# Kernel optimization log

Hardware: AMD Instinct MI355X
Metric: run time of the kernel (lower is better)

The kernel has to match this reference:

```python
import jax, jax.numpy as jnp
import numpy as np

D_MODEL = 256
NUM_HEADS = 4
HEAD_DIM = D_MODEL // NUM_HEADS


def setup_inputs() -> dict:
    key = jax.random.key(0)
    ks = jax.random.split(key, 16)
    B, N, M, C = 2, 256, 256, D_MODEL
    inp = {
        'q_tokens': jax.random.normal(ks[0], (B, N, C), jnp.float32),
        'k_tokens': jax.random.normal(ks[1], (B, M, C), jnp.float32),
        'v_tokens': jax.random.normal(ks[2], (B, M, C), jnp.float32),
        'qk_embeds': jax.random.normal(ks[3], (B, N, M, C), jnp.float32),
        'qv_embeds': jax.random.normal(ks[4], (B, N, M, C), jnp.float32),
    }
    scale = 1.0 / np.sqrt(C)
    # Linear layer params (weight used as x @ W + b)
    inp['Wq'] = jax.random.normal(ks[5], (C, C), jnp.float32) * scale
    inp['bq'] = jnp.zeros((C,), jnp.float32)
    inp['Wk'] = jax.random.normal(ks[6], (C, C), jnp.float32) * scale
    inp['bk'] = jnp.zeros((C,), jnp.float32)
    inp['Wv'] = jax.random.normal(ks[7], (C, C), jnp.float32) * scale
    inp['bv'] = jnp.zeros((C,), jnp.float32)
    inp['Wqk'] = jax.random.normal(ks[8], (C, C), jnp.float32) * scale
    inp['bqk'] = jnp.zeros((C,), jnp.float32)
    inp['Wqv'] = jax.random.normal(ks[9], (C, C), jnp.float32) * scale
    inp['bqv'] = jnp.zeros((C,), jnp.float32)
    return inp


def reference(q_tokens, k_tokens, v_tokens, qk_embeds, qv_embeds,
              Wq, bq, Wk, bk, Wv, bv, Wqk, bqk, Wqv, bqv):
    B, N, C = q_tokens.shape
    M = k_tokens.shape[1]
    H, hc = NUM_HEADS, HEAD_DIM

    # token projections -> (B, H, len, hc)
    q = (q_tokens @ Wq + bq).reshape(B, N, H, hc).transpose(0, 2, 1, 3)
    k = (k_tokens @ Wk + bk).reshape(B, M, H, hc).transpose(0, 2, 1, 3)
    v = (v_tokens @ Wv + bv).reshape(B, M, H, hc).transpose(0, 2, 1, 3)

    # pair-embedding projections -> (B, N, M, H, hc)
    qk = (qk_embeds @ Wqk + bqk).reshape(B, N, M, H, hc)
    qv = (qv_embeds @ Wqv + bqv).reshape(B, N, M, H, hc)

    # scores: q . (k + qk)  == q.k + q.qk
    scores = jnp.einsum('bhnc,bhmc->bhnm', q, k)
    scores = scores + jnp.einsum('bhnc,bnmhc->bhnm', q, qk)
    scores = scores / np.sqrt(hc).astype(np.float32)

    attn = jax.nn.softmax(scores, axis=-1)  # (B, H, N, M)

    # output: attn @ (v + qv) == attn@v + attn.qv
    hidden = jnp.einsum('bhnm,bhmc->bhnc', attn, v)
    hidden = hidden + jnp.einsum('bhnm,bnmhc->bhnc', attn, qv)
    hidden = hidden.transpose(0, 2, 1, 3).reshape(B, N, C)  # (B, N, C)
    return hidden, attn
```

## Files before the change

### kernel.cpp

```cpp
#include <hip/hip_runtime.h>

#define BB 2
#define NN 256
#define CC 256

__device__ __forceinline__ float dot4acc(float4 e, float4 w, float s) {
    s = fmaf(e.x, w.x, s); s = fmaf(e.y, w.y, s);
    s = fmaf(e.z, w.z, s); s = fmaf(e.w, w.w, s);
    return s;
}

__global__ __launch_bounds__(256) void proj_gemm(
    const float* __restrict__ q_tok, const float* __restrict__ k_tok, const float* __restrict__ v_tok,
    const float* __restrict__ Wq, const float* __restrict__ bq,
    const float* __restrict__ Wk, const float* __restrict__ bk,
    const float* __restrict__ Wv, const float* __restrict__ bv,
    float* __restrict__ out)
{
    const int row0 = blockIdx.x * 64;
    const int col0 = blockIdx.y * 64;
    const int seg  = row0 >> 9;
    const float* A    = seg == 0 ? q_tok : (seg == 1 ? k_tok : v_tok);
    const float* W    = seg == 0 ? Wq    : (seg == 1 ? Wk    : Wv);
    const float* bias = seg == 0 ? bq    : (seg == 1 ? bk    : bv);
    const int ar0 = row0 & 511;

    __shared__ float As[64][17];
    __shared__ float Bs[16][68];
    const int t  = threadIdx.x;
    const int tr = t >> 4, tc = t & 15;
    float acc[4][4] = {};

    const int sr  = t >> 2, sk4 = (t & 3) << 2;
    const int bkr = t >> 4, bj4 = (t & 15) << 2;

    for (int k0 = 0; k0 < 256; k0 += 16) {
        float4 a4 = *reinterpret_cast<const float4*>(&A[(ar0 + sr) * 256 + k0 + sk4]);
        float4 b4 = *reinterpret_cast<const float4*>(&W[(k0 + bkr) * 256 + col0 + bj4]);
        As[sr][sk4 + 0] = a4.x; As[sr][sk4 + 1] = a4.y; As[sr][sk4 + 2] = a4.z; As[sr][sk4 + 3] = a4.w;
        Bs[bkr][bj4 + 0] = b4.x; Bs[bkr][bj4 + 1] = b4.y; Bs[bkr][bj4 + 2] = b4.z; Bs[bkr][bj4 + 3] = b4.w;
        __syncthreads();
        #pragma unroll
        for (int k = 0; k < 16; ++k) {
            float a[4], bbv[4];
            #pragma unroll
            for (int i = 0; i < 4; ++i) a[i] = As[tr * 4 + i][k];
            #pragma unroll
            for (int j = 0; j < 4; ++j) bbv[j] = Bs[k][tc * 4 + j];
            #pragma unroll
            for (int i = 0; i < 4; ++i)
                #pragma unroll
                for (int j = 0; j < 4; ++j)
                    acc[i][j] = fmaf(a[i], bbv[j], acc[i][j]);
        }
        __syncthreads();
    }
    #pragma unroll
    for (int i = 0; i < 4; ++i) {
        const int r = row0 + tr * 4 + i;
        #pragma unroll
        for (int j = 0; j < 4; ++j) {
            const int cj = col0 + tc * 4 + j;
            out[r * 256 + cj] = acc[i][j] + bias[cj];
        }
    }
}

__global__ __launch_bounds__(256) void qw_gemm(
    const float* __restrict__ qp, const float* __restrict__ Wqk, float* __restrict__ qW)
{
    const int h    = blockIdx.z;
    const int row0 = blockIdx.x * 64;
    const int d0   = blockIdx.y * 64;
    __shared__ float As[64][17];
    __shared__ float Bs[16][68];
    const int t  = threadIdx.x;
    const int tr = t >> 4, tc = t & 15;
    float acc[4][4] = {};
    const int sr = t >> 2, sc4 = (t & 3) << 2;

    for (int k0 = 0; k0 < 64; k0 += 16) {
        float4 a4 = *reinterpret_cast<const float4*>(&qp[(row0 + sr) * 256 + h * 64 + k0 + sc4]);
        float4 b4 = *reinterpret_cast<const float4*>(&Wqk[(d0 + sr) * 256 + h * 64 + k0 + sc4]);
        As[sr][sc4 + 0] = a4.x; As[sr][sc4 + 1] = a4.y; As[sr][sc4 + 2] = a4.z; As[sr][sc4 + 3] = a4.w;
        Bs[sc4 + 0][sr] = b4.x; Bs[sc4 + 1][sr] = b4.y; Bs[sc4 + 2][sr] = b4.z; Bs[sc4 + 3][sr] = b4.w;
        __syncthreads();
        #pragma unroll
        for (int k = 0; k < 16; ++k) {
            float a[4], bbv[4];
            #pragma unroll
            for (int i = 0; i < 4; ++i) a[i] = As[tr * 4 + i][k];
            #pragma unroll
            for (int j = 0; j < 4; ++j) bbv[j] = Bs[k][tc * 4 + j];
            #pragma unroll
            for (int i = 0; i < 4; ++i)
                #pragma unroll
                for (int j = 0; j < 4; ++j)
                    acc[i][j] = fmaf(a[i], bbv[j], acc[i][j]);
        }
        __syncthreads();
    }
    #pragma unroll
    for (int i = 0; i < 4; ++i)
        #pragma unroll
        for (int j = 0; j < 4; ++j)
            qW[((row0 + tr * 4 + i) * 4 + h) * 256 + d0 + tc * 4 + j] = acc[i][j];
}

__global__ __launch_bounds__(256) void qk_gemm(
    const float* __restrict__ qkvp, float* __restrict__ Sqk)
{
    const int bh = blockIdx.z;
    const int b  = bh >> 2, h = bh & 3;
    const int n0 = blockIdx.x * 64;
    const int m0 = blockIdx.y * 64;
    __shared__ float As[64][17];
    __shared__ float Bs[16][68];
    const int t  = threadIdx.x;
    const int tr = t >> 4, tc = t & 15;
    float acc[4][4] = {};
    const int sr = t >> 2, sc4 = (t & 3) << 2;

    for (int k0 = 0; k0 < 64; k0 += 16) {
        float4 a4 = *reinterpret_cast<const float4*>(&qkvp[(size_t)(b * 256 + n0 + sr) * 256 + h * 64 + k0 + sc4]);
        float4 b4 = *reinterpret_cast<const float4*>(&qkvp[(size_t)(512 + b * 256 + m0 + sr) * 256 + h * 64 + k0 + sc4]);
        As[sr][sc4 + 0] = a4.x; As[sr][sc4 + 1] = a4.y; As[sr][sc4 + 2] = a4.z; As[sr][sc4 + 3] = a4.w;
        Bs[sc4 + 0][sr] = b4.x; Bs[sc4 + 1][sr] = b4.y; Bs[sc4 + 2][sr] = b4.z; Bs[sc4 + 3][sr] = b4.w;
        __syncthreads();
        #pragma unroll
        for (int k = 0; k < 16; ++k) {
            float a[4], bbv[4];
            #pragma unroll
            for (int i = 0; i < 4; ++i) a[i] = As[tr * 4 + i][k];
            #pragma unroll
            for (int j = 0; j < 4; ++j) bbv[j] = Bs[k][tc * 4 + j];
            #pragma unroll
            for (int i = 0; i < 4; ++i)
                #pragma unroll
                for (int j = 0; j < 4; ++j)
                    acc[i][j] = fmaf(a[i], bbv[j], acc[i][j]);
        }
        __syncthreads();
    }
    #pragma unroll
    for (int i = 0; i < 4; ++i)
        #pragma unroll
        for (int j = 0; j < 4; ++j)
            Sqk[(size_t)((b * 4 + h) * 256 + n0 + tr * 4 + i) * 256 + m0 + tc * 4 + j] = acc[i][j];
}


#define S1_LOAD(E00,E01,E02,E03,E10,E11,E12,E13, MB)                          \
    do {                                                                      \
        const float* _r0 = qk_emb + (size_t)(bn * 256 + (MB) + lr) * 256 + lq * 4; \
        const float* _r1 = _r0 + 1024;                                        \
        E00 = *reinterpret_cast<const float4*>(_r0);                          \
        E01 = *reinterpret_cast<const float4*>(_r0 + 64);                     \
        E02 = *reinterpret_cast<const float4*>(_r0 + 128);                    \
        E03 = *reinterpret_cast<const float4*>(_r0 + 192);                    \
        E10 = *reinterpret_cast<const float4*>(_r1);                          \
        E11 = *reinterpret_cast<const float4*>(_r1 + 64);                     \
        E12 = *reinterpret_cast<const float4*>(_r1 + 128);                    \
        E13 = *reinterpret_cast<const float4*>(_r1 + 192);                    \
    } while (0)

#define S1_COMP(E00,E01,E02,E03,E10,E11,E12,E13, MB)                          \
    do {                                                                      \
        const int _m0 = (MB) + lr;                                            \
        float p0[4], p1[4];                                                   \
        _Pragma("unroll")                                                     \
        for (int hh = 0; hh < 4; ++hh) {                                      \
            const float4 w0 = *reinterpret_cast<const float4*>(&qWs[hh * 256 + lq * 4]);        \
            const float4 w1 = *reinterpret_cast<const float4*>(&qWs[hh * 256 + 64 + lq * 4]);   \
            const float4 w2 = *reinterpret_cast<const float4*>(&qWs[hh * 256 + 128 + lq * 4]);  \
            const float4 w3 = *reinterpret_cast<const float4*>(&qWs[hh * 256 + 192 + lq * 4]);  \
            float s0 = 0.f, s1 = 0.f;                                         \
            s0 = dot4acc(E00, w0, s0); s0 = dot4acc(E01, w1, s0);             \
            s0 = dot4acc(E02, w2, s0); s0 = dot4acc(E03, w3, s0);             \
            s1 = dot4acc(E10, w0, s1); s1 = dot4acc(E11, w1, s1);             \
            s1 = dot4acc(E12, w2, s1); s1 = dot4acc(E13, w3, s1);             \
            p0[hh] = s0; p1[hh] = s1;                                         \
        }                                                                     \
        _Pragma("unroll")                                                     \
        for (int hh = 0; hh < 4; ++hh) {                                      \
            p0[hh] += __shfl_xor(p0[hh], 1); p1[hh] += __shfl_xor(p1[hh], 1); \
            p0[hh] += __shfl_xor(p0[hh], 2); p1[hh] += __shfl_xor(p1[hh], 2); \
            p0[hh] += __shfl_xor(p0[hh], 4); p1[hh] += __shfl_xor(p1[hh], 4); \
            p0[hh] += __shfl_xor(p0[hh], 8); p1[hh] += __shfl_xor(p1[hh], 8); \
        }                                                                     \
        if (lq == 0) {                                                        \
            _Pragma("unroll")                                                 \
            for (int hh = 0; hh < 4; ++hh) {                                  \
                Ssc[hh * 256 + _m0]     = p0[hh];                             \
                Ssc[hh * 256 + _m0 + 4] = p1[hh];                             \
            }                                                                 \
        }                                                                     \
    } while (0)

#define S2_LOAD(F0,F1,F2,F3,F4,F5,F6,F7, MB)                                  \
    do {                                                                      \
        const float* _rb = qv_emb + (size_t)(bn * 256 + (MB)) * 256 + l * 4;  \
        F0 = *reinterpret_cast<const float4*>(_rb);                           \
        F1 = *reinterpret_cast<const float4*>(_rb + 256);                     \
        F2 = *reinterpret_cast<const float4*>(_rb + 512);                     \
        F3 = *reinterpret_cast<const float4*>(_rb + 768);                     \
        F4 = *reinterpret_cast<const float4*>(_rb + 1024);                    \
        F5 = *reinterpret_cast<const float4*>(_rb + 1280);                    \
        F6 = *reinterpret_cast<const float4*>(_rb + 1536);                    \
        F7 = *reinterpret_cast<const float4*>(_rb + 1792);                    \
    } while (0)

#define S2_ONE(F, RIDX)                                                       \
    do {                                                                      \
        _Pragma("unroll")                                                     \
        for (int hh = 0; hh < 4; ++hh) {                                      \
            const float a = attn_s[hh * 256 + (RIDX)];                        \
            acc[hh].x = fmaf(a, F.x, acc[hh].x);                              \
            acc[hh].y = fmaf(a, F.y, acc[hh].y);                              \
            acc[hh].z = fmaf(a, F.z, acc[hh].z);                              \
            acc[hh].w = fmaf(a, F.w, acc[hh].w);                              \
        }                                                                     \
    } while (0)

#define S2_COMP(F0,F1,F2,F3,F4,F5,F6,F7, MB)                                  \
    do {                                                                      \
        S2_ONE(F0, (MB) + 0); S2_ONE(F1, (MB) + 1);                           \
        S2_ONE(F2, (MB) + 2); S2_ONE(F3, (MB) + 3);                           \
        S2_ONE(F4, (MB) + 4); S2_ONE(F5, (MB) + 5);                           \
        S2_ONE(F6, (MB) + 6); S2_ONE(F7, (MB) + 7);                           \
    } while (0)

__global__ __launch_bounds__(512, 4) void mega4(
    const float* __restrict__ qk_emb, const float* __restrict__ qv_emb,
    const float* __restrict__ qkvp, const float* __restrict__ qW,
    const float* __restrict__ Sqk, const float* __restrict__ Wqv,
    const float* __restrict__ bqv,
    float* __restrict__ attn_out, float* __restrict__ hidden)
{
    const int bn = blockIdx.x;
    const int b  = bn >> 8, n = bn & 255;
    const int t  = threadIdx.x;
    const int w  = t >> 6, l = t & 63;

    __shared__ float qWs[1024];
    __shared__ float SqkL[1024];
    __shared__ float Ssc[1024];
    __shared__ float attn_s[1024];
    __shared__ float Ap[4096];
    __shared__ float stage[16][256];
    __shared__ float pr[2][256];
    __shared__ float mxs[8][4], sums[8][4], scl[8][4];

    if (t < 256)
        *reinterpret_cast<float4*>(&qWs[t * 4]) =
            *reinterpret_cast<const float4*>(&qW[(size_t)bn * 1024 + t * 4]);
    __syncthreads();

    const int lq = l & 15, lr = l >> 4, li = l & 31;
    const int mw = w * 32;

    if (l < 32) {
        #pragma unroll
        for (int h = 0; h < 4; ++h)
            SqkL[h * 256 + mw + li] =
                Sqk[(size_t)((b * 4 + h) * 256 + n) * 256 + mw + li];
    }

    {
        float4 a00, a01, a02, a03, a10, a11, a12, a13;
        float4 b00, b01, b02, b03, b10, b11, b12, b13;
        S1_LOAD(a00,a01,a02,a03,a10,a11,a12,a13, mw + 0);
        S1_LOAD(b00,b01,b02,b03,b10,b11,b12,b13, mw + 8);
        S1_COMP(a00,a01,a02,a03,a10,a11,a12,a13, mw + 0);
        S1_LOAD(a00,a01,a02,a03,a10,a11,a12,a13, mw + 16);
        S1_COMP(b00,b01,b02,b03,b10,b11,b12,b13, mw + 8);
        S1_LOAD(b00,b01,b02,b03,b10,b11,b12,b13, mw + 24);
        S1_COMP(a00,a01,a02,a03,a10,a11,a12,a13, mw + 16);
        S1_COMP(b00,b01,b02,b03,b10,b11,b12,b13, mw + 24);
    }

    float mxw[4], smw[4];
    #pragma unroll
    for (int h = 0; h < 4; ++h) {
        const float sc = (Ssc[h * 256 + mw + li] + SqkL[h * 256 + mw + li]) * 0.125f;
        float mx = sc;
        #pragma unroll
        for (int mask = 16; mask >= 1; mask >>= 1) mx = fmaxf(mx, __shfl_xor(mx, mask));
        const float e = __expf(sc - mx);
        attn_s[h * 256 + mw + li] = e;
        float sm = e;
        #pragma unroll
        for (int mask = 16; mask >= 1; mask >>= 1) sm += __shfl_xor(sm, mask);
        mxw[h] = mx; smw[h] = sm;
    }
    if (l == 0) {
        #pragma unroll
        for (int h = 0; h < 4; ++h) { mxs[w][h] = mxw[h]; sums[w][h] = smw[h]; }
    }

    float4 acc[4];
    #pragma unroll
    for (int hh = 0; hh < 4; ++hh) acc[hh] = make_float4(0.f, 0.f, 0.f, 0.f);
    {
        float4 f0, f1, f2, f3, f4, f5, f6, f7;
        float4 g0, g1, g2, g3, g4, g5, g6, g7;
        S2_LOAD(f0,f1,f2,f3,f4,f5,f6,f7, mw + 0);
        S2_LOAD(g0,g1,g2,g3,g4,g5,g6,g7, mw + 8);
        S2_COMP(f0,f1,f2,f3,f4,f5,f6,f7, mw + 0);
        S2_LOAD(f0,f1,f2,f3,f4,f5,f6,f7, mw + 16);
        S2_COMP(g0,g1,g2,g3,g4,g5,g6,g7, mw + 8);
        S2_LOAD(g0,g1,g2,g3,g4,g5,g6,g7, mw + 24);
        S2_COMP(f0,f1,f2,f3,f4,f5,f6,f7, mw + 16);
        S2_COMP(g0,g1,g2,g3,g4,g5,g6,g7, mw + 24);
    }
    __syncthreads();

    if (t < 4) {
        const int h = t;
        float mg = mxs[0][h];
        #pragma unroll
        for (int ww = 1; ww < 8; ++ww) mg = fmaxf(mg, mxs[ww][h]);
        float sr[8]; float sg = 0.f;
        #pragma unroll
        for (int ww = 0; ww < 8; ++ww) { sr[ww] = __expf(mxs[ww][h] - mg); sg += sums[ww][h] * sr[ww]; }
        const float inv = 1.f / sg;
        #pragma unroll
        for (int ww = 0; ww < 8; ++ww) scl[ww][h] = sr[ww] * inv;
    }
    __syncthreads();

    {
        const int h = t >> 7, j = t & 127;
        float* ao = attn_out + (size_t)((b * 4 + h) * 256 + n) * 256;
        #pragma unroll
        for (int rep = 0; rep < 2; ++rep) {
            const int jj = j + rep * 128;
            const float a = attn_s[h * 256 + jj] * scl[jj >> 5][h];
            attn_s[h * 256 + jj] = a;
            ao[jj] = a;
        }
    }
    if (w < 4) {
        #pragma unroll
        for (int hh = 0; hh < 4; ++hh) {
            const float s = scl[w][hh];
            float4 v = acc[hh];
            v.x *= s; v.y *= s; v.z *= s; v.w *= s;
            *reinterpret_cast<float4*>(&Ap[(w * 4 + hh) * 256 + l * 4]) = v;
        }
    }
    __syncthreads();
    if (w >= 4) {
        #pragma unroll
        for (int hh = 0; hh < 4; ++hh) {
            const float s = scl[w][hh];
            float4* p = reinterpret_cast<float4*>(&Ap[((w - 4) * 4 + hh) * 256 + l * 4]);
            float4 o = *p;
            o.x = fmaf(acc[hh].x, s, o.x); o.y = fmaf(acc[hh].y, s, o.y);
            o.z = fmaf(acc[hh].z, s, o.z); o.w = fmaf(acc[hh].w, s, o.w);
            *p = o;
        }
    }
    __syncthreads();
    #pragma unroll
    for (int i = 0; i < 2; ++i) {
        const int idx = t + i * 512;
        const int hh = idx >> 8, d = idx & 255;
        Ap[hh * 256 + d] = Ap[hh * 256 + d] + Ap[(4 + hh) * 256 + d]
                         + Ap[(8 + hh) * 256 + d] + Ap[(12 + hh) * 256 + d];
    }

    {
        const int c = t & 255, half = t >> 8, hc = c >> 6;
        const int fr0 = t >> 6, fc0 = (t & 63) * 4;
        const int fr1 = fr0 + 8;
        const float* vbase = qkvp + (size_t)(1024 + b * 256) * 256;
        float4 ra = *reinterpret_cast<const float4*>(&vbase[(size_t)fr0 * 256 + fc0]);
        float4 rb = *reinterpret_cast<const float4*>(&vbase[(size_t)fr1 * 256 + fc0]);
        float hv = 0.f;
        for (int mt = 0; mt < 16; ++mt) {
            __syncthreads();
            *reinterpret_cast<float4*>(&stage[fr0][fc0]) = ra;
            *reinterpret_cast<float4*>(&stage[fr1][fc0]) = rb;
            if (mt < 15) {
                ra = *reinterpret_cast<const float4*>(&vbase[(size_t)((mt + 1) * 16 + fr0) * 256 + fc0]);
                rb = *reinterpret_cast<const float4*>(&vbase[(size_t)((mt + 1) * 16 + fr1) * 256 + fc0]);
            } else {
                ra = *reinterpret_cast<const float4*>(&Wqv[(size_t)fr0 * 256 + fc0]);
                rb = *reinterpret_cast<const float4*>(&Wqv[(size_t)fr1 * 256 + fc0]);
            }
            __syncthreads();
            #pragma unroll
            for (int r = 0; r < 8; ++r)
                hv = fmaf(attn_s[hc * 256 + mt * 16 + half * 8 + r], stage[half * 8 + r][c], hv);
        }
        for (int dt = 0; dt < 16; ++dt) {
            __syncthreads();
            *reinterpret_cast<float4*>(&stage[fr0][fc0]) = ra;
            *reinterpret_cast<float4*>(&stage[fr1][fc0]) = rb;
            if (dt < 15) {
                ra = *reinterpret_cast<const float4*>(&Wqv[(size_t)((dt + 1) * 16 + fr0) * 256 + fc0]);
                rb = *reinterpret_cast<const float4*>(&Wqv[(size_t)((dt + 1) * 16 + fr1) * 256 + fc0]);
            }
            __syncthreads();
            #pragma unroll
            for (int r = 0; r < 8; ++r)
                hv = fmaf(Ap[hc * 256 + dt * 16 + half * 8 + r], stage[half * 8 + r][c], hv);
        }
        pr[half][c] = hv;
    }
    __syncthreads();
    if (t < 256)
        hidden[(size_t)bn * 256 + t] = pr[0][t] + pr[1][t] + bqv[t];
}

extern "C" void kernel_launch(void* const* d_in, const int* in_sizes, int n_in,
                              void* d_out, int out_size, void* d_ws, size_t ws_size,
                              hipStream_t stream) {
    (void)in_sizes; (void)n_in; (void)out_size; (void)ws_size;
    const float* q_tok  = (const float*)d_in[0];
    const float* k_tok  = (const float*)d_in[1];
    const float* v_tok  = (const float*)d_in[2];
    const float* qk_emb = (const float*)d_in[3];
    const float* qv_emb = (const float*)d_in[4];
    const float* Wq  = (const float*)d_in[5];   const float* bq  = (const float*)d_in[6];
    const float* Wk  = (const float*)d_in[7];   const float* bk  = (const float*)d_in[8];
    const float* Wv  = (const float*)d_in[9];   const float* bv  = (const float*)d_in[10];
    const float* Wqk = (const float*)d_in[11];
    const float* Wqv = (const float*)d_in[13];  const float* bqv = (const float*)d_in[14];

    float* ws   = (float*)d_ws;
    float* qkvp = ws;
    float* qW   = ws + 393216;
    float* Sqk  = ws + 917504;

    float* hidden = (float*)d_out;
    float* attn   = (float*)d_out + BB * NN * CC;

    proj_gemm<<<dim3(24, 4),   256, 0, stream>>>(q_tok, k_tok, v_tok, Wq, bq, Wk, bk, Wv, bv, qkvp);
    qw_gemm  <<<dim3(8, 4, 4), 256, 0, stream>>>(qkvp, Wqk, qW);
    qk_gemm  <<<dim3(4, 4, 8), 256, 0, stream>>>(qkvp, Sqk);
    mega4    <<<512,           512, 0, stream>>>(qk_emb, qv_emb, qkvp, qW, Sqk, Wqv, bqv, attn, hidden);
}
```

Measured before the change: 91.64 us.

## Split per-row output projection out of mega kernel into a batched tiled GEMM

The per-row attn@v and Afull@Wqv products, which each block computed by streaming all of v and Wqv through shared memory, move into a separate tiled GEMM kernel. mega5 now writes the aggregated attention-weighted qv embeddings to workspace, and out_gemm reads them back. Softmax rescaling is recomputed per thread instead of through an extra barrier-separated stage, and the Ap reduction now covers all 8 waves at once. This removes redundant per-block reads of v/Wqv and several barriers, at the cost of an extra launch and a global round trip for Afull and attn.

```diff
diff --git a/kernel.cpp b/kernel.cpp
--- a/kernel.cpp
+++ b/kernel.cpp
@@ -188,12 +188,10 @@
             p0[hh] += __shfl_xor(p0[hh], 4); p1[hh] += __shfl_xor(p1[hh], 4); \
             p0[hh] += __shfl_xor(p0[hh], 8); p1[hh] += __shfl_xor(p1[hh], 8); \
         }                                                                     \
-        if (lq == 0) {                                                        \
-            _Pragma("unroll")                                                 \
-            for (int hh = 0; hh < 4; ++hh) {                                  \
-                Ssc[hh * 256 + _m0]     = p0[hh];                             \
-                Ssc[hh * 256 + _m0 + 4] = p1[hh];                             \
-            }                                                                 \
+        _Pragma("unroll")                                                     \
+        for (int hh = 0; hh < 4; ++hh) {                                      \
+            Ssc[hh * 256 + _m0]     = p0[hh];                                 \
+            Ssc[hh * 256 + _m0 + 4] = p1[hh];                                 \
         }                                                                     \
     } while (0)
 
@@ -230,12 +228,10 @@
         S2_ONE(F6, (MB) + 6); S2_ONE(F7, (MB) + 7);                           \
     } while (0)
 
-__global__ __launch_bounds__(512, 4) void mega4(
+__global__ __launch_bounds__(512, 4) void mega5(
     const float* __restrict__ qk_emb, const float* __restrict__ qv_emb,
-    const float* __restrict__ qkvp, const float* __restrict__ qW,
-    const float* __restrict__ Sqk, const float* __restrict__ Wqv,
-    const float* __restrict__ bqv,
-    float* __restrict__ attn_out, float* __restrict__ hidden)
+    const float* __restrict__ qW, const float* __restrict__ Sqk,
+    float* __restrict__ attn_out, float* __restrict__ Afull_g)
 {
     const int bn = blockIdx.x;
     const int b  = bn >> 8, n = bn & 255;
@@ -246,25 +242,21 @@
     __shared__ float SqkL[1024];
     __shared__ float Ssc[1024];
     __shared__ float attn_s[1024];
-    __shared__ float Ap[4096];
-    __shared__ float stage[16][256];
-    __shared__ float pr[2][256];
-    __shared__ float mxs[8][4], sums[8][4], scl[8][4];
-
-    if (t < 256)
-        *reinterpret_cast<float4*>(&qWs[t * 4]) =
-            *reinterpret_cast<const float4*>(&qW[(size_t)bn * 1024 + t * 4]);
+    __shared__ float Ap[8192];
+    __shared__ float mxs[8][4], sums[8][4];
+
+    {
+        const int i2 = t * 2;
+        *reinterpret_cast<float2*>(&qWs[i2]) =
+            *reinterpret_cast<const float2*>(&qW[(size_t)bn * 1024 + i2]);
+        const int h = i2 >> 8, m = i2 & 255;
+        *reinterpret_cast<float2*>(&SqkL[i2]) =
+            *reinterpret_cast<const float2*>(&Sqk[(size_t)((b * 4 + h) * 256 + n) * 256 + m]);
+    }
     __syncthreads();
 
     const int lq = l & 15, lr = l >> 4, li = l & 31;
     const int mw = w * 32;
-
-    if (l < 32) {
-        #pragma unroll
-        for (int h = 0; h < 4; ++h)
-            SqkL[h * 256 + mw + li] =
-                Sqk[(size_t)((b * 4 + h) * 256 + n) * 256 + mw + li];
-    }
 
     {
         float4 a00, a01, a02, a03, a10, a11, a12, a13;
@@ -279,7 +271,6 @@
         S1_COMP(b00,b01,b02,b03,b10,b11,b12,b13, mw + 24);
     }
 
-    float mxw[4], smw[4];
     #pragma unroll
     for (int h = 0; h < 4; ++h) {
         const float sc = (Ssc[h * 256 + mw + li] + SqkL[h * 256 + mw + li]) * 0.125f;
@@ -291,11 +282,8 @@
         float sm = e;
         #pragma unroll
         for (int mask = 16; mask >= 1; mask >>= 1) sm += __shfl_xor(sm, mask);
-        mxw[h] = mx; smw[h] = sm;
-    }
-    if (l == 0) {
-        #pragma unroll
-        for (int h = 0; h < 4; ++h) { mxs[w][h] = mxw[h]; sums[w][h] = smw[h]; }
+        mxs[w][h]  = mx;
+        sums[w][h] = sm;
     }
 
     float4 acc[4];
@@ -315,19 +303,17 @@
     }
     __syncthreads();
 
-    if (t < 4) {
-        const int h = t;
+    float mgv[4], invv[4];
+    #pragma unroll
+    for (int h = 0; h < 4; ++h) {
         float mg = mxs[0][h];
         #pragma unroll
         for (int ww = 1; ww < 8; ++ww) mg = fmaxf(mg, mxs[ww][h]);
-        float sr[8]; float sg = 0.f;
-        #pragma unroll
-        for (int ww = 0; ww < 8; ++ww) { sr[ww] = __expf(mxs[ww][h] - mg); sg += sums[ww][h] * sr[ww]; }
-        const float inv = 1.f / sg;
-        #pragma unroll
-        for (int ww = 0; ww < 8; ++ww) scl[ww][h] = sr[ww] * inv;
-    }
-    __syncthreads();
+        float sg = 0.f;
+        #pragma unroll
+        for (int ww = 0; ww < 8; ++ww) sg += sums[ww][h] * __expf(mxs[ww][h] - mg);
+        mgv[h] = mg; invv[h] = 1.f / sg;
+    }
 
     {
         const int h = t >> 7, j = t & 127;
@@ -335,83 +321,102 @@
         #pragma unroll
         for (int rep = 0; rep < 2; ++rep) {
             const int jj = j + rep * 128;
-            const float a = attn_s[h * 256 + jj] * scl[jj >> 5][h];
-            attn_s[h * 256 + jj] = a;
-            ao[jj] = a;
-        }
-    }
-    if (w < 4) {
-        #pragma unroll
-        for (int hh = 0; hh < 4; ++hh) {
-            const float s = scl[w][hh];
-            float4 v = acc[hh];
-            v.x *= s; v.y *= s; v.z *= s; v.w *= s;
-            *reinterpret_cast<float4*>(&Ap[(w * 4 + hh) * 256 + l * 4]) = v;
-        }
+            const float s = __expf(mxs[jj >> 5][h] - mgv[h]) * invv[h];
+            ao[jj] = attn_s[h * 256 + jj] * s;
+        }
+    }
+
+    #pragma unroll
+    for (int hh = 0; hh < 4; ++hh) {
+        const float s = __expf(mxs[w][hh] - mgv[hh]) * invv[hh];
+        float4 v = acc[hh];
+        v.x *= s; v.y *= s; v.z *= s; v.w *= s;
+        *reinterpret_cast<float4*>(&Ap[(w * 4 + hh) * 256 + l * 4]) = v;
     }
     __syncthreads();
-    if (w >= 4) {
-        #pragma unroll
-        for (int hh = 0; hh < 4; ++hh) {
-            const float s = scl[w][hh];
-            float4* p = reinterpret_cast<float4*>(&Ap[((w - 4) * 4 + hh) * 256 + l * 4]);
-            float4 o = *p;
-            o.x = fmaf(acc[hh].x, s, o.x); o.y = fmaf(acc[hh].y, s, o.y);
-            o.z = fmaf(acc[hh].z, s, o.z); o.w = fmaf(acc[hh].w, s, o.w);
-            *p = o;
-        }
-    }
-    __syncthreads();
+
     #pragma unroll
     for (int i = 0; i < 2; ++i) {
         const int idx = t + i * 512;
         const int hh = idx >> 8, d = idx & 255;
-        Ap[hh * 256 + d] = Ap[hh * 256 + d] + Ap[(4 + hh) * 256 + d]
-                         + Ap[(8 + hh) * 256 + d] + Ap[(12 + hh) * 256 + d];
-    }
-
-    {
-        const int c = t & 255, half = t >> 8, hc = c >> 6;
-        const int fr0 = t >> 6, fc0 = (t & 63) * 4;
-        const int fr1 = fr0 + 8;
-        const float* vbase = qkvp + (size_t)(1024 + b * 256) * 256;
-        float4 ra = *reinterpret_cast<const float4*>(&vbase[(size_t)fr0 * 256 + fc0]);
-        float4 rb = *reinterpret_cast<const float4*>(&vbase[(size_t)fr1 * 256 + fc0]);
-        float hv = 0.f;
-        for (int mt = 0; mt < 16; ++mt) {
-            __syncthreads();
-            *reinterpret_cast<float4*>(&stage[fr0][fc0]) = ra;
-            *reinterpret_cast<float4*>(&stage[fr1][fc0]) = rb;
-            if (mt < 15) {
-                ra = *reinterpret_cast<const float4*>(&vbase[(size_t)((mt + 1) * 16 + fr0) * 256 + fc0]);
-                rb = *reinterpret_cast<const float4*>(&vbase[(size_t)((mt + 1) * 16 + fr1) * 256 + fc0]);
-            } else {
-                ra = *reinterpret_cast<const float4*>(&Wqv[(size_t)fr0 * 256 + fc0]);
-                rb = *reinterpret_cast<const float4*>(&Wqv[(size_t)fr1 * 256 + fc0]);
-            }
-            __syncthreads();
-            #pragma unroll
-            for (int r = 0; r < 8; ++r)
-                hv = fmaf(attn_s[hc * 256 + mt * 16 + half * 8 + r], stage[half * 8 + r][c], hv);
-        }
-        for (int dt = 0; dt < 16; ++dt) {
-            __syncthreads();
-            *reinterpret_cast<float4*>(&stage[fr0][fc0]) = ra;
-            *reinterpret_cast<float4*>(&stage[fr1][fc0]) = rb;
-            if (dt < 15) {
-                ra = *reinterpret_cast<const float4*>(&Wqv[(size_t)((dt + 1) * 16 + fr0) * 256 + fc0]);
-                rb = *reinterpret_cast<const float4*>(&Wqv[(size_t)((dt + 1) * 16 + fr1) * 256 + fc0]);
-            }
-            __syncthreads();
-            #pragma unroll
-            for (int r = 0; r < 8; ++r)
-                hv = fmaf(Ap[hc * 256 + dt * 16 + half * 8 + r], stage[half * 8 + r][c], hv);
-        }
-        pr[half][c] = hv;
-    }
-    __syncthreads();
-    if (t < 256)
-        hidden[(size_t)bn * 256 + t] = pr[0][t] + pr[1][t] + bqv[t];
+        float s = 0.f;
+        #pragma unroll
+        for (int ww = 0; ww < 8; ++ww) s += Ap[(ww * 4 + hh) * 256 + d];
+        Afull_g[(size_t)bn * 1024 + hh * 256 + d] = s;
+    }
+}
+
+__global__ __launch_bounds__(256) void out_gemm(
+    const float* __restrict__ qkvp, const float* __restrict__ attn,
+    const float* __restrict__ Afull, const float* __restrict__ Wqv,
+    const float* __restrict__ bqv, float* __restrict__ hidden)
+{
+    const int h  = blockIdx.y;
+    const int r0 = blockIdx.x * 64;
+    const int b  = r0 >> 8;
+    __shared__ float As[64][17];
+    __shared__ float Bs[16][68];
+    const int t  = threadIdx.x;
+    const int tr = t >> 4, tc = t & 15;
+    const int sr = t >> 2, sk4 = (t & 3) << 2;
+    const int bkr = t >> 4, bj4 = (t & 15) << 2;
+    float acc[4][4] = {};
+
+    for (int k0 = 0; k0 < 256; k0 += 16) {
+        float4 a4 = *reinterpret_cast<const float4*>(
+            &attn[(size_t)((b * 4 + h) * 256 + ((r0 + sr) & 255)) * 256 + k0 + sk4]);
+        float4 b4 = *reinterpret_cast<const float4*>(
+            &qkvp[(size_t)(1024 + b * 256 + k0 + bkr) * 256 + h * 64 + bj4]);
+        As[sr][sk4 + 0] = a4.x; As[sr][sk4 + 1] = a4.y; As[sr][sk4 + 2] = a4.z; As[sr][sk4 + 3] = a4.w;
+        Bs[bkr][bj4 + 0] = b4.x; Bs[bkr][bj4 + 1] = b4.y; Bs[bkr][bj4 + 2] = b4.z; Bs[bkr][bj4 + 3] = b4.w;
+        __syncthreads();
+        #pragma unroll
+        for (int k = 0; k < 16; ++k) {
+            float a[4], bbv[4];
+            #pragma unroll
+            for (int i = 0; i < 4; ++i) a[i] = As[tr * 4 + i][k];
+            #pragma unroll
+            for (int j = 0; j < 4; ++j) bbv[j] = Bs[k][tc * 4 + j];
+            #pragma unroll
+            for (int i = 0; i < 4; ++i)
+                #pragma unroll
+                for (int j = 0; j < 4; ++j)
+                    acc[i][j] = fmaf(a[i], bbv[j], acc[i][j]);
+        }
+        __syncthreads();
+    }
+    for (int k0 = 0; k0 < 256; k0 += 16) {
+        float4 a4 = *reinterpret_cast<const float4*>(
+            &Afull[(size_t)(r0 + sr) * 1024 + h * 256 + k0 + sk4]);
+        float4 b4 = *reinterpret_cast<const float4*>(
+            &Wqv[(size_t)(k0 + bkr) * 256 + h * 64 + bj4]);
+        As[sr][sk4 + 0] = a4.x; As[sr][sk4 + 1] = a4.y; As[sr][sk4 + 2] = a4.z; As[sr][sk4 + 3] = a4.w;
+        Bs[bkr][bj4 + 0] = b4.x; Bs[bkr][bj4 + 1] = b4.y; Bs[bkr][bj4 + 2] = b4.z; Bs[bkr][bj4 + 3] = b4.w;
+        __syncthreads();
+        #pragma unroll
+        for (int k = 0; k < 16; ++k) {
+            float a[4], bbv[4];
+            #pragma unroll
+            for (int i = 0; i < 4; ++i) a[i] = As[tr * 4 + i][k];
+            #pragma unroll
+            for (int j = 0; j < 4; ++j) bbv[j] = Bs[k][tc * 4 + j];
+            #pragma unroll
+            for (int i = 0; i < 4; ++i)
+                #pragma unroll
+                for (int j = 0; j < 4; ++j)
+                    acc[i][j] = fmaf(a[i], bbv[j], acc[i][j]);
+        }
+        __syncthreads();
+    }
+    #pragma unroll
+    for (int i = 0; i < 4; ++i) {
+        const int r = r0 + tr * 4 + i;
+        #pragma unroll
+        for (int j = 0; j < 4; ++j) {
+            const int cj = h * 64 + tc * 4 + j;
+            hidden[(size_t)r * 256 + cj] = acc[i][j] + bqv[cj];
+        }
+    }
 }
 
 extern "C" void kernel_launch(void* const* d_in, const int* in_sizes, int n_in,
@@ -429,10 +434,11 @@
     const float* Wqk = (const float*)d_in[11];
     const float* Wqv = (const float*)d_in[13];  const float* bqv = (const float*)d_in[14];
 
-    float* ws   = (float*)d_ws;
-    float* qkvp = ws;
-    float* qW   = ws + 393216;
-    float* Sqk  = ws + 917504;
+    float* ws    = (float*)d_ws;
+    float* qkvp  = ws;
+    float* qW    = ws + 393216;
+    float* Sqk   = ws + 917504;
+    float* Afull = ws + 1441792;
 
     float* hidden = (float*)d_out;
     float* attn   = (float*)d_out + BB * NN * CC;
@@ -440,5 +446,6 @@
     proj_gemm<<<dim3(24, 4),   256, 0, stream>>>(q_tok, k_tok, v_tok, Wq, bq, Wk, bk, Wv, bv, qkvp);
     qw_gemm  <<<dim3(8, 4, 4), 256, 0, stream>>>(qkvp, Wqk, qW);
     qk_gemm  <<<dim3(4, 4, 8), 256, 0, stream>>>(qkvp, Sqk);
-    mega4    <<<512,           512, 0, stream>>>(qk_emb, qv_emb, qkvp, qW, Sqk, Wqv, bqv, attn, hidden);
-}
+    mega5    <<<512,           512, 0, stream>>>(qk_emb, qv_emb, qW, Sqk, attn, Afull);
+    out_gemm <<<dim3(8, 4),    256, 0, stream>>>(qkvp, attn, Afull, Wqv, bqv, hidden);
+}
```

Measured after the change: 154.4 us. 1.68x slower.
